# Performance work log

Hardware: AMD Instinct MI355X
Metric: run time of the kernel (lower is better)

The kernel has to match this reference:

```python
import jax, jax.numpy as jnp
import numpy as np

H = 4      # num_heads
C = 64     # attention_num_c
C_Z = 128  # num_in_c (pair rep channels)
C_T = 64   # num_in_c_kv (template pair channels)


def setup_inputs() -> dict:
    key = jax.random.key(0)
    ks = jax.random.split(key, 7)
    B, T, R = 1, 4, 384
    z2d = jax.random.normal(ks[0], (B, R, R, C_Z), dtype=jnp.float32)
    t2d = jax.random.normal(ks[1], (B, T, R, R, C_T), dtype=jnp.float32)
    s = 0.02
    Wq = jax.random.normal(ks[2], (C_Z, H * C), dtype=jnp.float32) * s
    Wk = jax.random.normal(ks[3], (C_T, H * C), dtype=jnp.float32) * s
    Wv = jax.random.normal(ks[4], (C_T, H * C), dtype=jnp.float32) * s
    Wo = jax.random.normal(ks[5], (H * C, C_Z), dtype=jnp.float32) * s
    bo = jax.random.normal(ks[6], (C_Z,), dtype=jnp.float32) * s
    return {"z2d": z2d, "t2d": t2d, "Wq": Wq, "Wk": Wk, "Wv": Wv, "Wo": Wo, "bo": bo}


def reference(z2d, t2d, Wq, Wk, Wv, Wo, bo):
    B, R = z2d.shape[0], z2d.shape[-2]
    T = t2d.shape[1]
    P = R * R  # residue-pair axis
    # query: one query per residue pair
    zq = z2d.reshape(B, P, 1, C_Z)
    # templates become the key/value axis per residue pair
    tkv = jnp.transpose(t2d, (0, 2, 3, 1, 4)).reshape(B, P, T, C_T)
    q = (zq @ Wq).reshape(B, P, 1, H, C) * (C ** -0.5)
    k = (tkv @ Wk).reshape(B, P, T, H, C)
    v = (tkv @ Wv).reshape(B, P, T, H, C)
    logits = jnp.einsum('bpqhc,bpkhc->bphqk', q, k)  # [B,P,H,1,T]
    weights = jax.nn.softmax(logits, axis=-1)
    weighted_avg = jnp.einsum('bphqk,bpkhc->bpqhc', weights, v)  # [B,P,1,H,C]
    out = weighted_avg.reshape(B, P, 1, H * C) @ Wo + bo
    return out.reshape(B, R, R, C_Z)
```

## Files before the change

kernel.cpp:

```cpp
#include <hip/hip_runtime.h>


#define R_   384
#define P_   (R_ * R_)
#define NBLK (P_ / 64)

typedef __attribute__((ext_vector_type(8))) short  short8;
typedef __attribute__((ext_vector_type(4))) float  f32x4;

__device__ __forceinline__ unsigned short f2bf(float f) {
  unsigned u = __float_as_uint(f);
  unsigned r = ((u >> 16) & 1u) + 0x7FFFu;
  return (unsigned short)((u + r) >> 16);
}
__device__ __forceinline__ float bf2f(unsigned short s) {
  return __uint_as_float(((unsigned)s) << 16);
}
__device__ __forceinline__ int swz(int p, int c) {
  return p * 256 + ((((c >> 3) ^ (p & 31)) << 3) | (c & 7));
}

__global__ void prep_kernel(const float* __restrict__ Wq, const float* __restrict__ Wk,
                            const float* __restrict__ Wv, const float* __restrict__ Wo,
                            unsigned short* __restrict__ AbarT,
                            unsigned short* __restrict__ MbarT) {
  int tid = blockIdx.x * blockDim.x + threadIdx.x;
  if (tid < 256 * 128) {
    int n = tid >> 7, i = tid & 127;
    int h = n >> 6, j = n & 63;
    const float* wq = Wq + i * 256 + h * 64;
    const float* wk = Wk + j * 256 + h * 64;
    float acc = 0.f;
#pragma unroll 8
    for (int c = 0; c < 64; ++c) acc += wq[c] * wk[c];
    AbarT[n * 128 + i] = f2bf(acc * 0.125f);
  } else {
    int t2 = tid - 256 * 128;
    int o = t2 >> 8, k = t2 & 255;
    int h = k >> 6, j = k & 63;
    const float* wv = Wv + j * 256 + h * 64;
    const float* wo = Wo + (h * 64) * 128 + o;
    float acc = 0.f;
#pragma unroll 8
    for (int c = 0; c < 64; ++c) acc += wv[c] * wo[c * 128];
    MbarT[o * 256 + k] = f2bf(acc);
  }
}

__global__ __launch_bounds__(256, 2) void attn_kernel(
    const float* __restrict__ z2d, const float* __restrict__ t2d,
    const unsigned short* __restrict__ AbarT, const unsigned short* __restrict__ MbarT,
    const float* __restrict__ bo, float* __restrict__ out) {
  __shared__ __align__(16) unsigned short sT[64 * 256];
  __shared__ __align__(16) unsigned short sG[64 * 256];

  const int tid = threadIdx.x;
  const int P0  = blockIdx.x * 64;

#pragma unroll
  for (int it = 0; it < 16; ++it) {
    int f  = it * 256 + tid;
    int t  = f >> 10;
    int rr = f & 1023;
    int p  = rr >> 4;
    int j4 = (rr & 15) << 2;
    const float4 v = *(const float4*)(t2d + (size_t)(t * P_ + P0 + p) * 64 + j4);
    ushort4 pk;
    pk.x = f2bf(v.x); pk.y = f2bf(v.y); pk.z = f2bf(v.z); pk.w = f2bf(v.w);
    *(ushort4*)(sT + swz(p, t * 64 + j4)) = pk;
  }

  const int wv_  = tid >> 6;
  const int lane = tid & 63;
  const int l = lane & 15;
  const int q = lane >> 4;

  f32x4 acc[16];
#pragma unroll
  for (int i = 0; i < 16; ++i) acc[i] = f32x4{0.f, 0.f, 0.f, 0.f};
  const float* zrow = z2d + (size_t)(P0 + wv_ * 16 + l) * 128;
#pragma unroll
  for (int kk = 0; kk < 4; ++kk) {
    float4 za = *(const float4*)(zrow + kk * 32 + q * 8);
    float4 zb = *(const float4*)(zrow + kk * 32 + q * 8 + 4);
    short8 af;
    af[0] = (short)f2bf(za.x); af[1] = (short)f2bf(za.y);
    af[2] = (short)f2bf(za.z); af[3] = (short)f2bf(za.w);
    af[4] = (short)f2bf(zb.x); af[5] = (short)f2bf(zb.y);
    af[6] = (short)f2bf(zb.z); af[7] = (short)f2bf(zb.w);
    const unsigned short* bbase = AbarT + l * 128 + kk * 32 + q * 8;
#pragma unroll
    for (int nt = 0; nt < 16; ++nt) {
      short8 bf = *(const short8*)(bbase + nt * 2048);
      acc[nt] = __builtin_amdgcn_mfma_f32_16x16x32_bf16(af, bf, acc[nt], 0, 0, 0);
    }
  }
#pragma unroll
  for (int nt = 0; nt < 16; ++nt) {
    int c = nt * 16 + l;
#pragma unroll
    for (int r = 0; r < 4; ++r) {
      int p = wv_ * 16 + q * 4 + r;
      sG[swz(p, c)] = f2bf(acc[nt][r]);
    }
  }
  __syncthreads();

  {
    const int p = tid & 63;
    const int h = tid >> 6;
    float lg0 = 0.f, lg1 = 0.f, lg2 = 0.f, lg3 = 0.f;
#pragma unroll
    for (int jb = 0; jb < 64; jb += 4) {
      ushort4 g4 = *(const ushort4*)(sG + swz(p, h * 64 + jb));
      float g0 = bf2f(g4.x), g1 = bf2f(g4.y), g2 = bf2f(g4.z), g3 = bf2f(g4.w);
      ushort4 k0 = *(const ushort4*)(sT + swz(p, jb));
      ushort4 k1 = *(const ushort4*)(sT + swz(p, 64 + jb));
      ushort4 k2 = *(const ushort4*)(sT + swz(p, 128 + jb));
      ushort4 k3 = *(const ushort4*)(sT + swz(p, 192 + jb));
      lg0 += g0 * bf2f(k0.x) + g1 * bf2f(k0.y) + g2 * bf2f(k0.z) + g3 * bf2f(k0.w);
      lg1 += g0 * bf2f(k1.x) + g1 * bf2f(k1.y) + g2 * bf2f(k1.z) + g3 * bf2f(k1.w);
      lg2 += g0 * bf2f(k2.x) + g1 * bf2f(k2.y) + g2 * bf2f(k2.z) + g3 * bf2f(k2.w);
      lg3 += g0 * bf2f(k3.x) + g1 * bf2f(k3.y) + g2 * bf2f(k3.z) + g3 * bf2f(k3.w);
    }
    float mx = fmaxf(fmaxf(lg0, lg1), fmaxf(lg2, lg3));
    float e0 = __expf(lg0 - mx), e1 = __expf(lg1 - mx);
    float e2 = __expf(lg2 - mx), e3 = __expf(lg3 - mx);
    float inv = 1.f / (e0 + e1 + e2 + e3);
    e0 *= inv; e1 *= inv; e2 *= inv; e3 *= inv;
#pragma unroll
    for (int jb = 0; jb < 64; jb += 4) {
      ushort4 k0 = *(const ushort4*)(sT + swz(p, jb));
      ushort4 k1 = *(const ushort4*)(sT + swz(p, 64 + jb));
      ushort4 k2 = *(const ushort4*)(sT + swz(p, 128 + jb));
      ushort4 k3 = *(const ushort4*)(sT + swz(p, 192 + jb));
      ushort4 sv;
      sv.x = f2bf(e0 * bf2f(k0.x) + e1 * bf2f(k1.x) + e2 * bf2f(k2.x) + e3 * bf2f(k3.x));
      sv.y = f2bf(e0 * bf2f(k0.y) + e1 * bf2f(k1.y) + e2 * bf2f(k2.y) + e3 * bf2f(k3.y));
      sv.z = f2bf(e0 * bf2f(k0.z) + e1 * bf2f(k1.z) + e2 * bf2f(k2.z) + e3 * bf2f(k3.z));
      sv.w = f2bf(e0 * bf2f(k0.w) + e1 * bf2f(k1.w) + e2 * bf2f(k2.w) + e3 * bf2f(k3.w));
      *(ushort4*)(sG + swz(p, h * 64 + jb)) = sv;
    }
  }
  __syncthreads();

  f32x4 acc2[4][2];
#pragma unroll
  for (int mt = 0; mt < 4; ++mt) {
    acc2[mt][0] = f32x4{0.f, 0.f, 0.f, 0.f};
    acc2[mt][1] = f32x4{0.f, 0.f, 0.f, 0.f};
  }
#pragma unroll
  for (int kk = 0; kk < 8; ++kk) {
    const unsigned short* mb = MbarT + (size_t)(wv_ * 32 + l) * 256 + kk * 32 + q * 8;
    short8 b0 = *(const short8*)(mb);
    short8 b1 = *(const short8*)(mb + 16 * 256);
#pragma unroll
    for (int mt = 0; mt < 4; ++mt) {
      const int p  = mt * 16 + l;
      const int cb = kk * 32 + q * 8;
      short8 af2 = *(const short8*)(sG + p * 256 + (((cb >> 3) ^ (p & 31)) << 3));
      acc2[mt][0] = __builtin_amdgcn_mfma_f32_16x16x32_bf16(af2, b0, acc2[mt][0], 0, 0, 0);
      acc2[mt][1] = __builtin_amdgcn_mfma_f32_16x16x32_bf16(af2, b1, acc2[mt][1], 0, 0, 0);
    }
  }
  const float bo0 = bo[wv_ * 32 + l];
  const float bo1 = bo[wv_ * 32 + 16 + l];
#pragma unroll
  for (int mt = 0; mt < 4; ++mt) {
#pragma unroll
    for (int r = 0; r < 4; ++r) {
      size_t row = (size_t)(P0 + mt * 16 + q * 4 + r);
      out[row * 128 + wv_ * 32 + l]      = acc2[mt][0][r] + bo0;
      out[row * 128 + wv_ * 32 + 16 + l] = acc2[mt][1][r] + bo1;
    }
  }
}

extern "C" void kernel_launch(void* const* d_in, const int* in_sizes, int n_in,
                              void* d_out, int out_size, void* d_ws, size_t ws_size,
                              hipStream_t stream) {
  const float* z2d = (const float*)d_in[0];
  const float* t2d = (const float*)d_in[1];
  const float* Wq  = (const float*)d_in[2];
  const float* Wk  = (const float*)d_in[3];
  const float* Wv  = (const float*)d_in[4];
  const float* Wo  = (const float*)d_in[5];
  const float* bo  = (const float*)d_in[6];

  unsigned short* AbarT = (unsigned short*)d_ws;
  unsigned short* MbarT = AbarT + 256 * 128;
  float* out = (float*)d_out;

  hipLaunchKernelGGL(prep_kernel, dim3(256), dim3(256), 0, stream,
                     Wq, Wk, Wv, Wo, AbarT, MbarT);
  hipLaunchKernelGGL(attn_kernel, dim3(NBLK), dim3(256), 0, stream,
                     z2d, t2d, AbarT, MbarT, bo, out);
}
```

Before: 354.9 us.

## Halve per-block pair tile to 32 and remap waves for higher occupancy

Each block now handles 32 residue pairs instead of 64, which halves shared memory and accumulator registers so launch bounds can request four blocks per CU. The wave-to-tile mapping in both MFMA GEMMs is rearranged so each wave covers one 16-row M tile and half the N dimension. The softmax stage splits each pair's channel reduction across two lanes, using 16-byte LDS accesses and a shuffle to combine partial sums. In exchange, the weight matrices are reread from global/L2 by twice as many blocks, and there is more per-block overhead.

```diff
diff --git a/kernel.cpp b/kernel.cpp
--- a/kernel.cpp
+++ b/kernel.cpp
@@ -3,7 +3,8 @@
 
 #define R_   384
 #define P_   (R_ * R_)
-#define NBLK (P_ / 64)
+#define PB   32
+#define NBLK (P_ / PB)
 
 typedef __attribute__((ext_vector_type(8))) short  short8;
 typedef __attribute__((ext_vector_type(4))) float  f32x4;
@@ -47,21 +48,21 @@
   }
 }
 
-__global__ __launch_bounds__(256, 2) void attn_kernel(
+__global__ __launch_bounds__(256, 4) void attn_kernel(
     const float* __restrict__ z2d, const float* __restrict__ t2d,
     const unsigned short* __restrict__ AbarT, const unsigned short* __restrict__ MbarT,
     const float* __restrict__ bo, float* __restrict__ out) {
-  __shared__ __align__(16) unsigned short sT[64 * 256];
-  __shared__ __align__(16) unsigned short sG[64 * 256];
+  __shared__ __align__(16) unsigned short sT[PB * 256];
+  __shared__ __align__(16) unsigned short sG[PB * 256];
 
   const int tid = threadIdx.x;
-  const int P0  = blockIdx.x * 64;
-
-#pragma unroll
-  for (int it = 0; it < 16; ++it) {
+  const int P0  = blockIdx.x * PB;
+
+#pragma unroll
+  for (int it = 0; it < 8; ++it) {
     int f  = it * 256 + tid;
-    int t  = f >> 10;
-    int rr = f & 1023;
+    int t  = f >> 9;
+    int rr = f & 511;
     int p  = rr >> 4;
     int j4 = (rr & 15) << 2;
     const float4 v = *(const float4*)(t2d + (size_t)(t * P_ + P0 + p) * 64 + j4);
@@ -74,11 +75,13 @@
   const int lane = tid & 63;
   const int l = lane & 15;
   const int q = lane >> 4;
-
-  f32x4 acc[16];
-#pragma unroll
-  for (int i = 0; i < 16; ++i) acc[i] = f32x4{0.f, 0.f, 0.f, 0.f};
-  const float* zrow = z2d + (size_t)(P0 + wv_ * 16 + l) * 128;
+  const int mt = wv_ & 1;
+  const int nh = wv_ >> 1;
+
+  f32x4 acc[8];
+#pragma unroll
+  for (int i = 0; i < 8; ++i) acc[i] = f32x4{0.f, 0.f, 0.f, 0.f};
+  const float* zrow = z2d + (size_t)(P0 + mt * 16 + l) * 128;
 #pragma unroll
   for (int kk = 0; kk < 4; ++kk) {
     float4 za = *(const float4*)(zrow + kk * 32 + q * 8);
@@ -88,91 +91,98 @@
     af[2] = (short)f2bf(za.z); af[3] = (short)f2bf(za.w);
     af[4] = (short)f2bf(zb.x); af[5] = (short)f2bf(zb.y);
     af[6] = (short)f2bf(zb.z); af[7] = (short)f2bf(zb.w);
-    const unsigned short* bbase = AbarT + l * 128 + kk * 32 + q * 8;
-#pragma unroll
-    for (int nt = 0; nt < 16; ++nt) {
-      short8 bf = *(const short8*)(bbase + nt * 2048);
-      acc[nt] = __builtin_amdgcn_mfma_f32_16x16x32_bf16(af, bf, acc[nt], 0, 0, 0);
-    }
-  }
-#pragma unroll
-  for (int nt = 0; nt < 16; ++nt) {
-    int c = nt * 16 + l;
+    const unsigned short* bbase = AbarT + (nh * 8) * 2048 + l * 128 + kk * 32 + q * 8;
+#pragma unroll
+    for (int i = 0; i < 8; ++i) {
+      short8 bf = *(const short8*)(bbase + i * 2048);
+      acc[i] = __builtin_amdgcn_mfma_f32_16x16x32_bf16(af, bf, acc[i], 0, 0, 0);
+    }
+  }
+#pragma unroll
+  for (int i = 0; i < 8; ++i) {
+    int c = (nh * 8 + i) * 16 + l;
 #pragma unroll
     for (int r = 0; r < 4; ++r) {
-      int p = wv_ * 16 + q * 4 + r;
-      sG[swz(p, c)] = f2bf(acc[nt][r]);
+      int p = mt * 16 + q * 4 + r;
+      sG[swz(p, c)] = f2bf(acc[i][r]);
     }
   }
   __syncthreads();
 
   {
-    const int p = tid & 63;
-    const int h = tid >> 6;
+    const int p    = lane >> 1;
+    const int half = lane & 1;
+    const int h    = wv_;
+    const int c0   = half * 32;
     float lg0 = 0.f, lg1 = 0.f, lg2 = 0.f, lg3 = 0.f;
 #pragma unroll
-    for (int jb = 0; jb < 64; jb += 4) {
-      ushort4 g4 = *(const ushort4*)(sG + swz(p, h * 64 + jb));
-      float g0 = bf2f(g4.x), g1 = bf2f(g4.y), g2 = bf2f(g4.z), g3 = bf2f(g4.w);
-      ushort4 k0 = *(const ushort4*)(sT + swz(p, jb));
-      ushort4 k1 = *(const ushort4*)(sT + swz(p, 64 + jb));
-      ushort4 k2 = *(const ushort4*)(sT + swz(p, 128 + jb));
-      ushort4 k3 = *(const ushort4*)(sT + swz(p, 192 + jb));
-      lg0 += g0 * bf2f(k0.x) + g1 * bf2f(k0.y) + g2 * bf2f(k0.z) + g3 * bf2f(k0.w);
-      lg1 += g0 * bf2f(k1.x) + g1 * bf2f(k1.y) + g2 * bf2f(k1.z) + g3 * bf2f(k1.w);
-      lg2 += g0 * bf2f(k2.x) + g1 * bf2f(k2.y) + g2 * bf2f(k2.z) + g3 * bf2f(k2.w);
-      lg3 += g0 * bf2f(k3.x) + g1 * bf2f(k3.y) + g2 * bf2f(k3.z) + g3 * bf2f(k3.w);
-    }
+    for (int jj = 0; jj < 4; ++jj) {
+      const int cc = c0 + jj * 8;
+      short8 g8 = *(const short8*)(sG + swz(p, h * 64 + cc));
+      short8 k0 = *(const short8*)(sT + swz(p, cc));
+      short8 k1 = *(const short8*)(sT + swz(p, 64 + cc));
+      short8 k2 = *(const short8*)(sT + swz(p, 128 + cc));
+      short8 k3 = *(const short8*)(sT + swz(p, 192 + cc));
+#pragma unroll
+      for (int e = 0; e < 8; ++e) {
+        float g = bf2f((unsigned short)g8[e]);
+        lg0 += g * bf2f((unsigned short)k0[e]);
+        lg1 += g * bf2f((unsigned short)k1[e]);
+        lg2 += g * bf2f((unsigned short)k2[e]);
+        lg3 += g * bf2f((unsigned short)k3[e]);
+      }
+    }
+    lg0 += __shfl_xor(lg0, 1);
+    lg1 += __shfl_xor(lg1, 1);
+    lg2 += __shfl_xor(lg2, 1);
+    lg3 += __shfl_xor(lg3, 1);
     float mx = fmaxf(fmaxf(lg0, lg1), fmaxf(lg2, lg3));
     float e0 = __expf(lg0 - mx), e1 = __expf(lg1 - mx);
     float e2 = __expf(lg2 - mx), e3 = __expf(lg3 - mx);
     float inv = 1.f / (e0 + e1 + e2 + e3);
     e0 *= inv; e1 *= inv; e2 *= inv; e3 *= inv;
 #pragma unroll
-    for (int jb = 0; jb < 64; jb += 4) {
-      ushort4 k0 = *(const ushort4*)(sT + swz(p, jb));
-      ushort4 k1 = *(const ushort4*)(sT + swz(p, 64 + jb));
-      ushort4 k2 = *(const ushort4*)(sT + swz(p, 128 + jb));
-      ushort4 k3 = *(const ushort4*)(sT + swz(p, 192 + jb));
-      ushort4 sv;
-      sv.x = f2bf(e0 * bf2f(k0.x) + e1 * bf2f(k1.x) + e2 * bf2f(k2.x) + e3 * bf2f(k3.x));
-      sv.y = f2bf(e0 * bf2f(k0.y) + e1 * bf2f(k1.y) + e2 * bf2f(k2.y) + e3 * bf2f(k3.y));
-      sv.z = f2bf(e0 * bf2f(k0.z) + e1 * bf2f(k1.z) + e2 * bf2f(k2.z) + e3 * bf2f(k3.z));
-      sv.w = f2bf(e0 * bf2f(k0.w) + e1 * bf2f(k1.w) + e2 * bf2f(k2.w) + e3 * bf2f(k3.w));
-      *(ushort4*)(sG + swz(p, h * 64 + jb)) = sv;
+    for (int jj = 0; jj < 4; ++jj) {
+      const int cc = c0 + jj * 8;
+      short8 k0 = *(const short8*)(sT + swz(p, cc));
+      short8 k1 = *(const short8*)(sT + swz(p, 64 + cc));
+      short8 k2 = *(const short8*)(sT + swz(p, 128 + cc));
+      short8 k3 = *(const short8*)(sT + swz(p, 192 + cc));
+      short8 sv;
+#pragma unroll
+      for (int e = 0; e < 8; ++e) {
+        float s = e0 * bf2f((unsigned short)k0[e]) + e1 * bf2f((unsigned short)k1[e])
+                + e2 * bf2f((unsigned short)k2[e]) + e3 * bf2f((unsigned short)k3[e]);
+        sv[e] = (short)f2bf(s);
+      }
+      *(short8*)(sG + swz(p, h * 64 + cc)) = sv;
     }
   }
   __syncthreads();
 
-  f32x4 acc2[4][2];
-#pragma unroll
-  for (int mt = 0; mt < 4; ++mt) {
-    acc2[mt][0] = f32x4{0.f, 0.f, 0.f, 0.f};
-    acc2[mt][1] = f32x4{0.f, 0.f, 0.f, 0.f};
-  }
+  f32x4 acc2[4];
+#pragma unroll
+  for (int i = 0; i < 4; ++i) acc2[i] = f32x4{0.f, 0.f, 0.f, 0.f};
 #pragma unroll
   for (int kk = 0; kk < 8; ++kk) {
-    const unsigned short* mb = MbarT + (size_t)(wv_ * 32 + l) * 256 + kk * 32 + q * 8;
-    short8 b0 = *(const short8*)(mb);
-    short8 b1 = *(const short8*)(mb + 16 * 256);
-#pragma unroll
-    for (int mt = 0; mt < 4; ++mt) {
-      const int p  = mt * 16 + l;
-      const int cb = kk * 32 + q * 8;
-      short8 af2 = *(const short8*)(sG + p * 256 + (((cb >> 3) ^ (p & 31)) << 3));
-      acc2[mt][0] = __builtin_amdgcn_mfma_f32_16x16x32_bf16(af2, b0, acc2[mt][0], 0, 0, 0);
-      acc2[mt][1] = __builtin_amdgcn_mfma_f32_16x16x32_bf16(af2, b1, acc2[mt][1], 0, 0, 0);
-    }
-  }
-  const float bo0 = bo[wv_ * 32 + l];
-  const float bo1 = bo[wv_ * 32 + 16 + l];
-#pragma unroll
-  for (int mt = 0; mt < 4; ++mt) {
+    const int p  = mt * 16 + l;
+    const int cb = kk * 32 + q * 8;
+    short8 af2 = *(const short8*)(sG + p * 256 + (((cb >> 3) ^ (p & 31)) << 3));
+    const unsigned short* mb = MbarT + (size_t)(nh * 64 + l) * 256 + kk * 32 + q * 8;
+#pragma unroll
+    for (int i = 0; i < 4; ++i) {
+      short8 bf = *(const short8*)(mb + i * 16 * 256);
+      acc2[i] = __builtin_amdgcn_mfma_f32_16x16x32_bf16(af2, bf, acc2[i], 0, 0, 0);
+    }
+  }
+#pragma unroll
+  for (int i = 0; i < 4; ++i) {
+    const int o   = nh * 64 + i * 16 + l;
+    const float b = bo[o];
 #pragma unroll
     for (int r = 0; r < 4; ++r) {
       size_t row = (size_t)(P0 + mt * 16 + q * 4 + r);
-      out[row * 128 + wv_ * 32 + l]      = acc2[mt][0][r] + bo0;
-      out[row * 128 + wv_ * 32 + 16 + l] = acc2[mt][1][r] + bo1;
+      out[row * 128 + o] = acc2[i][r] + b;
     }
   }
 }
```

Result: slower. 394.4 us (+11.1%).

## Convert attention kernel to persistent blocks with double-buffered software pipeline

Applied to the files above, without the earlier changes.

Replaces the one-tile-per-block launch with 256 persistent 512-thread blocks, each looping over 18 tiles of 32 pairs. Abar is staged once in LDS and the Mbar fragments are held in registers, so per-tile weight reloads from global memory go away. Each iteration prefetches the next tile's t2d and z2d into registers and overlaps the previous tile's output GEMM with the current tile's work through double-buffered LDS. It also uses packed bf16 conversion instructions, wider LDS accesses with shuffle reductions, and 128KB of dynamic shared memory, which raises register pressure and may limit occupancy.

```diff
diff --git a/kernel.cpp b/kernel.cpp
--- a/kernel.cpp
+++ b/kernel.cpp
@@ -1,12 +1,16 @@
 #include <hip/hip_runtime.h>
 
 
-#define R_   384
-#define P_   (R_ * R_)
-#define NBLK (P_ / 64)
+#define R_    384
+#define P_    (R_ * R_)
+#define PB    32
+#define NPB   256
+#define NT_   18
 
 typedef __attribute__((ext_vector_type(8))) short  short8;
 typedef __attribute__((ext_vector_type(4))) float  f32x4;
+
+union S8U { short8 s8; unsigned u[4]; };
 
 __device__ __forceinline__ unsigned short f2bf(float f) {
   unsigned u = __float_as_uint(f);
@@ -16,9 +20,18 @@
 __device__ __forceinline__ float bf2f(unsigned short s) {
   return __uint_as_float(((unsigned)s) << 16);
 }
+__device__ __forceinline__ unsigned cvtpk(float lo, float hi) {
+  unsigned d;
+  asm("v_cvt_pk_bf16_f32 %0, %1, %2" : "=v"(d) : "v"(lo), "v"(hi));
+  return d;
+}
 __device__ __forceinline__ int swz(int p, int c) {
   return p * 256 + ((((c >> 3) ^ (p & 31)) << 3) | (c & 7));
 }
+#define BAR() do { \
+    asm volatile("s_waitcnt lgkmcnt(0)\ns_barrier" ::: "memory"); \
+    __builtin_amdgcn_sched_barrier(0); \
+  } while (0)
 
 __global__ void prep_kernel(const float* __restrict__ Wq, const float* __restrict__ Wk,
                             const float* __restrict__ Wv, const float* __restrict__ Wo,
@@ -47,134 +60,221 @@
   }
 }
 
-__global__ __launch_bounds__(256, 2) void attn_kernel(
+__global__ __launch_bounds__(512, 2) void attn_kernel(
     const float* __restrict__ z2d, const float* __restrict__ t2d,
     const unsigned short* __restrict__ AbarT, const unsigned short* __restrict__ MbarT,
     const float* __restrict__ bo, float* __restrict__ out) {
-  __shared__ __align__(16) unsigned short sT[64 * 256];
-  __shared__ __align__(16) unsigned short sG[64 * 256];
-
-  const int tid = threadIdx.x;
-  const int P0  = blockIdx.x * 64;
-
-#pragma unroll
-  for (int it = 0; it < 16; ++it) {
-    int f  = it * 256 + tid;
-    int t  = f >> 10;
-    int rr = f & 1023;
-    int p  = rr >> 4;
-    int j4 = (rr & 15) << 2;
-    const float4 v = *(const float4*)(t2d + (size_t)(t * P_ + P0 + p) * 64 + j4);
-    ushort4 pk;
-    pk.x = f2bf(v.x); pk.y = f2bf(v.y); pk.z = f2bf(v.z); pk.w = f2bf(v.w);
-    *(ushort4*)(sT + swz(p, t * 64 + j4)) = pk;
-  }
-
+  extern __shared__ unsigned short smem[];
+  unsigned short* sAbar = smem;
+  unsigned short* sT    = smem + 32768;
+  unsigned short* sG    = smem + 49152;
+
+  const int tid  = threadIdx.x;
   const int wv_  = tid >> 6;
   const int lane = tid & 63;
   const int l = lane & 15;
   const int q = lane >> 4;
-
-  f32x4 acc[16];
-#pragma unroll
-  for (int i = 0; i < 16; ++i) acc[i] = f32x4{0.f, 0.f, 0.f, 0.f};
-  const float* zrow = z2d + (size_t)(P0 + wv_ * 16 + l) * 128;
-#pragma unroll
-  for (int kk = 0; kk < 4; ++kk) {
-    float4 za = *(const float4*)(zrow + kk * 32 + q * 8);
-    float4 zb = *(const float4*)(zrow + kk * 32 + q * 8 + 4);
-    short8 af;
-    af[0] = (short)f2bf(za.x); af[1] = (short)f2bf(za.y);
-    af[2] = (short)f2bf(za.z); af[3] = (short)f2bf(za.w);
-    af[4] = (short)f2bf(zb.x); af[5] = (short)f2bf(zb.y);
-    af[6] = (short)f2bf(zb.z); af[7] = (short)f2bf(zb.w);
-    const unsigned short* bbase = AbarT + l * 128 + kk * 32 + q * 8;
-#pragma unroll
-    for (int nt = 0; nt < 16; ++nt) {
-      short8 bf = *(const short8*)(bbase + nt * 2048);
-      acc[nt] = __builtin_amdgcn_mfma_f32_16x16x32_bf16(af, bf, acc[nt], 0, 0, 0);
-    }
-  }
-#pragma unroll
-  for (int nt = 0; nt < 16; ++nt) {
-    int c = nt * 16 + l;
+  const int mt = wv_ & 1;
+  const int ng = wv_ >> 1;
+
+  int sOffS[4], sOffD[4];
+#pragma unroll
+  for (int k2 = 0; k2 < 4; ++k2) {
+    int f = k2 * 512 + tid, t = f >> 9, rr = f & 511;
+    int p2 = rr >> 4, j4 = (rr & 15) << 2;
+    sOffS[k2] = t * (P_ * 64) + p2 * 64 + j4;
+    sOffD[k2] = swz(p2, t * 64 + j4);
+  }
+  const int zoff = (mt * 16 + l) * 128;
+  const int p2g  = mt * 16 + l;
+  const int ap = tid >> 4, asub = tid & 15;
+  const int ah = asub >> 2, au = asub & 3;
+  const int aoG0 = swz(ap, ah * 64 + au * 16);
+  const int aoG1 = swz(ap, ah * 64 + au * 16 + 8);
+  int aoK[4][2];
+#pragma unroll
+  for (int t = 0; t < 4; ++t) {
+    aoK[t][0] = swz(ap, t * 64 + au * 16);
+    aoK[t][1] = swz(ap, t * 64 + au * 16 + 8);
+  }
+
+#pragma unroll
+  for (int k2 = 0; k2 < 8; ++k2) {
+    int id = k2 * 512 + tid, n = id >> 4, blk = id & 15;
+    short8 v = *(const short8*)(AbarT + n * 128 + blk * 8);
+    *(short8*)(sAbar + n * 128 + ((blk ^ (n & 15)) << 3)) = v;
+  }
+  short8 mb0[8], mb1[8];
+#pragma unroll
+  for (int kk = 0; kk < 8; ++kk) {
+    mb0[kk] = *(const short8*)(MbarT + (size_t)((ng * 2)     * 16 + l) * 256 + kk * 32 + q * 8);
+    mb1[kk] = *(const short8*)(MbarT + (size_t)((ng * 2 + 1) * 16 + l) * 256 + kk * 32 + q * 8);
+  }
+  const float bo0 = bo[(ng * 2) * 16 + l];
+  const float bo1 = bo[(ng * 2 + 1) * 16 + l];
+
+  float4 st0, st1, st2, st3;
+  float4 zpA[8], zpB[8];
+  {
+    const size_t P00 = (size_t)blockIdx.x * PB;
+    const float* tb = t2d + P00 * 64;
+    st0 = *(const float4*)(tb + sOffS[0]);
+    st1 = *(const float4*)(tb + sOffS[1]);
+    st2 = *(const float4*)(tb + sOffS[2]);
+    st3 = *(const float4*)(tb + sOffS[3]);
+    const float* zr = z2d + P00 * 128 + zoff;
+#pragma unroll
+    for (int kk = 0; kk < 4; ++kk) {
+      zpA[2 * kk]     = *(const float4*)(zr + kk * 32 + q * 8);
+      zpA[2 * kk + 1] = *(const float4*)(zr + kk * 32 + q * 8 + 4);
+    }
+  }
+  BAR();
+
+  auto gemm2 = [&](const unsigned short* sGp, size_t P0p) {
+    f32x4 a20 = f32x4{0.f, 0.f, 0.f, 0.f};
+    f32x4 a21 = f32x4{0.f, 0.f, 0.f, 0.f};
+#pragma unroll
+    for (int kk = 0; kk < 8; ++kk) {
+      short8 af2 = *(const short8*)(sGp + p2g * 256 + (((kk * 4 + q) ^ (p2g & 31)) << 3));
+      a20 = __builtin_amdgcn_mfma_f32_16x16x32_bf16(af2, mb0[kk], a20, 0, 0, 0);
+      a21 = __builtin_amdgcn_mfma_f32_16x16x32_bf16(af2, mb1[kk], a21, 0, 0, 0);
+    }
+    const size_t rb = (P0p + (size_t)(mt * 16 + q * 4)) * 128;
 #pragma unroll
     for (int r = 0; r < 4; ++r) {
-      int p = wv_ * 16 + q * 4 + r;
-      sG[swz(p, c)] = f2bf(acc[nt][r]);
-    }
-  }
-  __syncthreads();
-
-  {
-    const int p = tid & 63;
-    const int h = tid >> 6;
+      out[rb + r * 128 + ng * 32 + l]      = a20[r] + bo0;
+      out[rb + r * 128 + ng * 32 + 16 + l] = a21[r] + bo1;
+    }
+  };
+
+  auto attention = [&](const unsigned short* sTc, unsigned short* sGc) {
+    short8 g0 = *(const short8*)(sGc + aoG0);
+    short8 g1 = *(const short8*)(sGc + aoG1);
+    short8 kc00 = *(const short8*)(sTc + aoK[0][0]);
+    short8 kc01 = *(const short8*)(sTc + aoK[0][1]);
+    short8 kc10 = *(const short8*)(sTc + aoK[1][0]);
+    short8 kc11 = *(const short8*)(sTc + aoK[1][1]);
+    short8 kc20 = *(const short8*)(sTc + aoK[2][0]);
+    short8 kc21 = *(const short8*)(sTc + aoK[2][1]);
+    short8 kc30 = *(const short8*)(sTc + aoK[3][0]);
+    short8 kc31 = *(const short8*)(sTc + aoK[3][1]);
     float lg0 = 0.f, lg1 = 0.f, lg2 = 0.f, lg3 = 0.f;
 #pragma unroll
-    for (int jb = 0; jb < 64; jb += 4) {
-      ushort4 g4 = *(const ushort4*)(sG + swz(p, h * 64 + jb));
-      float g0 = bf2f(g4.x), g1 = bf2f(g4.y), g2 = bf2f(g4.z), g3 = bf2f(g4.w);
-      ushort4 k0 = *(const ushort4*)(sT + swz(p, jb));
-      ushort4 k1 = *(const ushort4*)(sT + swz(p, 64 + jb));
-      ushort4 k2 = *(const ushort4*)(sT + swz(p, 128 + jb));
-      ushort4 k3 = *(const ushort4*)(sT + swz(p, 192 + jb));
-      lg0 += g0 * bf2f(k0.x) + g1 * bf2f(k0.y) + g2 * bf2f(k0.z) + g3 * bf2f(k0.w);
-      lg1 += g0 * bf2f(k1.x) + g1 * bf2f(k1.y) + g2 * bf2f(k1.z) + g3 * bf2f(k1.w);
-      lg2 += g0 * bf2f(k2.x) + g1 * bf2f(k2.y) + g2 * bf2f(k2.z) + g3 * bf2f(k2.w);
-      lg3 += g0 * bf2f(k3.x) + g1 * bf2f(k3.y) + g2 * bf2f(k3.z) + g3 * bf2f(k3.w);
-    }
-    float mx = fmaxf(fmaxf(lg0, lg1), fmaxf(lg2, lg3));
+    for (int e = 0; e < 8; ++e) {
+      const float ga = bf2f((unsigned short)g0[e]);
+      const float gb = bf2f((unsigned short)g1[e]);
+      lg0 += ga * bf2f((unsigned short)kc00[e]) + gb * bf2f((unsigned short)kc01[e]);
+      lg1 += ga * bf2f((unsigned short)kc10[e]) + gb * bf2f((unsigned short)kc11[e]);
+      lg2 += ga * bf2f((unsigned short)kc20[e]) + gb * bf2f((unsigned short)kc21[e]);
+      lg3 += ga * bf2f((unsigned short)kc30[e]) + gb * bf2f((unsigned short)kc31[e]);
+    }
+    lg0 += __shfl_xor(lg0, 1); lg0 += __shfl_xor(lg0, 2);
+    lg1 += __shfl_xor(lg1, 1); lg1 += __shfl_xor(lg1, 2);
+    lg2 += __shfl_xor(lg2, 1); lg2 += __shfl_xor(lg2, 2);
+    lg3 += __shfl_xor(lg3, 1); lg3 += __shfl_xor(lg3, 2);
+    const float mx = fmaxf(fmaxf(lg0, lg1), fmaxf(lg2, lg3));
     float e0 = __expf(lg0 - mx), e1 = __expf(lg1 - mx);
     float e2 = __expf(lg2 - mx), e3 = __expf(lg3 - mx);
-    float inv = 1.f / (e0 + e1 + e2 + e3);
+    const float inv = 1.f / (e0 + e1 + e2 + e3);
     e0 *= inv; e1 *= inv; e2 *= inv; e3 *= inv;
-#pragma unroll
-    for (int jb = 0; jb < 64; jb += 4) {
-      ushort4 k0 = *(const ushort4*)(sT + swz(p, jb));
-      ushort4 k1 = *(const ushort4*)(sT + swz(p, 64 + jb));
-      ushort4 k2 = *(const ushort4*)(sT + swz(p, 128 + jb));
-      ushort4 k3 = *(const ushort4*)(sT + swz(p, 192 + jb));
-      ushort4 sv;
-      sv.x = f2bf(e0 * bf2f(k0.x) + e1 * bf2f(k1.x) + e2 * bf2f(k2.x) + e3 * bf2f(k3.x));
-      sv.y = f2bf(e0 * bf2f(k0.y) + e1 * bf2f(k1.y) + e2 * bf2f(k2.y) + e3 * bf2f(k3.y));
-      sv.z = f2bf(e0 * bf2f(k0.z) + e1 * bf2f(k1.z) + e2 * bf2f(k2.z) + e3 * bf2f(k3.z));
-      sv.w = f2bf(e0 * bf2f(k0.w) + e1 * bf2f(k1.w) + e2 * bf2f(k2.w) + e3 * bf2f(k3.w));
-      *(ushort4*)(sG + swz(p, h * 64 + jb)) = sv;
-    }
-  }
-  __syncthreads();
-
-  f32x4 acc2[4][2];
-#pragma unroll
-  for (int mt = 0; mt < 4; ++mt) {
-    acc2[mt][0] = f32x4{0.f, 0.f, 0.f, 0.f};
-    acc2[mt][1] = f32x4{0.f, 0.f, 0.f, 0.f};
-  }
-#pragma unroll
-  for (int kk = 0; kk < 8; ++kk) {
-    const unsigned short* mb = MbarT + (size_t)(wv_ * 32 + l) * 256 + kk * 32 + q * 8;
-    short8 b0 = *(const short8*)(mb);
-    short8 b1 = *(const short8*)(mb + 16 * 256);
-#pragma unroll
-    for (int mt = 0; mt < 4; ++mt) {
-      const int p  = mt * 16 + l;
-      const int cb = kk * 32 + q * 8;
-      short8 af2 = *(const short8*)(sG + p * 256 + (((cb >> 3) ^ (p & 31)) << 3));
-      acc2[mt][0] = __builtin_amdgcn_mfma_f32_16x16x32_bf16(af2, b0, acc2[mt][0], 0, 0, 0);
-      acc2[mt][1] = __builtin_amdgcn_mfma_f32_16x16x32_bf16(af2, b1, acc2[mt][1], 0, 0, 0);
-    }
-  }
-  const float bo0 = bo[wv_ * 32 + l];
-  const float bo1 = bo[wv_ * 32 + 16 + l];
-#pragma unroll
-  for (int mt = 0; mt < 4; ++mt) {
-#pragma unroll
-    for (int r = 0; r < 4; ++r) {
-      size_t row = (size_t)(P0 + mt * 16 + q * 4 + r);
-      out[row * 128 + wv_ * 32 + l]      = acc2[mt][0][r] + bo0;
-      out[row * 128 + wv_ * 32 + 16 + l] = acc2[mt][1][r] + bo1;
-    }
-  }
+    S8U sv;
+#pragma unroll
+    for (int j2 = 0; j2 < 4; ++j2) {
+      float s0 = e0 * bf2f((unsigned short)kc00[2 * j2])     + e1 * bf2f((unsigned short)kc10[2 * j2])
+               + e2 * bf2f((unsigned short)kc20[2 * j2])     + e3 * bf2f((unsigned short)kc30[2 * j2]);
+      float s1 = e0 * bf2f((unsigned short)kc00[2 * j2 + 1]) + e1 * bf2f((unsigned short)kc10[2 * j2 + 1])
+               + e2 * bf2f((unsigned short)kc20[2 * j2 + 1]) + e3 * bf2f((unsigned short)kc30[2 * j2 + 1]);
+      sv.u[j2] = cvtpk(s0, s1);
+    }
+    *(short8*)(sGc + aoG0) = sv.s8;
+#pragma unroll
+    for (int j2 = 0; j2 < 4; ++j2) {
+      float s0 = e0 * bf2f((unsigned short)kc01[2 * j2])     + e1 * bf2f((unsigned short)kc11[2 * j2])
+               + e2 * bf2f((unsigned short)kc21[2 * j2])     + e3 * bf2f((unsigned short)kc31[2 * j2]);
+      float s1 = e0 * bf2f((unsigned short)kc01[2 * j2 + 1]) + e1 * bf2f((unsigned short)kc11[2 * j2 + 1])
+               + e2 * bf2f((unsigned short)kc21[2 * j2 + 1]) + e3 * bf2f((unsigned short)kc31[2 * j2 + 1]);
+      sv.u[j2] = cvtpk(s0, s1);
+    }
+    *(short8*)(sGc + aoG1) = sv.s8;
+  };
+
+#define HALF_BODY(IT_, CUR_, ZPC, ZPN, DO_G2, DO_PF)                           \
+  {                                                                            \
+    const size_t P0 = (size_t)blockIdx.x * PB + (size_t)(IT_) * (NPB * PB);    \
+    unsigned short* sTc = sT + (CUR_) * 8192;                                  \
+    unsigned short* sGc = sG + (CUR_) * 8192;                                  \
+    const unsigned short* sGp = sG + (1 - (CUR_)) * 8192;                      \
+                \
+    { uint2 w;                                                                 \
+      w.x = cvtpk(st0.x, st0.y); w.y = cvtpk(st0.z, st0.w);                    \
+      *(uint2*)(sTc + sOffD[0]) = w;                                           \
+      w.x = cvtpk(st1.x, st1.y); w.y = cvtpk(st1.z, st1.w);                    \
+      *(uint2*)(sTc + sOffD[1]) = w;                                           \
+      w.x = cvtpk(st2.x, st2.y); w.y = cvtpk(st2.z, st2.w);                    \
+      *(uint2*)(sTc + sOffD[2]) = w;                                           \
+      w.x = cvtpk(st3.x, st3.y); w.y = cvtpk(st3.z, st3.w);                    \
+      *(uint2*)(sTc + sOffD[3]) = w; }                                         \
+    \
+    if (DO_PF) {                                                               \
+      const float* tb = t2d + (P0 + NPB * PB) * 64;                            \
+      st0 = *(const float4*)(tb + sOffS[0]);                                   \
+      st1 = *(const float4*)(tb + sOffS[1]);                                   \
+      st2 = *(const float4*)(tb + sOffS[2]);                                   \
+      st3 = *(const float4*)(tb + sOffS[3]);                                   \
+      const float* zr = z2d + (P0 + NPB * PB) * 128 + zoff;                    \
+      _Pragma("unroll")                                                        \
+      for (int kk = 0; kk < 4; ++kk) {                                         \
+        ZPN[2 * kk]     = *(const float4*)(zr + kk * 32 + q * 8);              \
+        ZPN[2 * kk + 1] = *(const float4*)(zr + kk * 32 + q * 8 + 4);          \
+      }                                                                        \
+    }                                                                          \
+                                                  \
+    if (DO_G2) gemm2(sGp, P0 - (size_t)(NPB * PB));                            \
+                   \
+    {                                                                          \
+      f32x4 a1[4];                                                             \
+      _Pragma("unroll")                                                        \
+      for (int i = 0; i < 4; ++i) a1[i] = f32x4{0.f, 0.f, 0.f, 0.f};           \
+      _Pragma("unroll")                                                        \
+      for (int kk = 0; kk < 4; ++kk) {                                         \
+        S8U af;                                                                \
+        af.u[0] = cvtpk(ZPC[2 * kk].x,     ZPC[2 * kk].y);                     \
+        af.u[1] = cvtpk(ZPC[2 * kk].z,     ZPC[2 * kk].w);                     \
+        af.u[2] = cvtpk(ZPC[2 * kk + 1].x, ZPC[2 * kk + 1].y);                 \
+        af.u[3] = cvtpk(ZPC[2 * kk + 1].z, ZPC[2 * kk + 1].w);                 \
+        _Pragma("unroll")                                                      \
+        for (int i = 0; i < 4; ++i) {                                          \
+          const int n = (ng * 4 + i) * 16 + l;                                 \
+          short8 bf = *(const short8*)(sAbar + n * 128 + (((kk * 4 + q) ^ l) << 3)); \
+          a1[i] = __builtin_amdgcn_mfma_f32_16x16x32_bf16(af.s8, bf, a1[i], 0, 0, 0); \
+        }                                                                      \
+      }                                                                        \
+      _Pragma("unroll")                                                        \
+      for (int i = 0; i < 4; ++i) {                                            \
+        const int c = (ng * 4 + i) * 16 + l;                                   \
+        _Pragma("unroll")                                                      \
+        for (int r = 0; r < 4; ++r) {                                          \
+          const int p2 = mt * 16 + q * 4 + r;                                  \
+          sGc[swz(p2, c)] = f2bf(a1[i][r]);    \
+        }                                                                      \
+      }                                                                        \
+    }                                                                          \
+    BAR();                                                                     \
+                                                    \
+    attention(sTc, sGc);                                                       \
+    BAR();                                                                     \
+  }
+
+#pragma unroll 1
+  for (int j = 0; j < NT_ / 2; ++j) {
+    const int it0 = 2 * j;
+    HALF_BODY(it0,     0, zpA, zpB, (it0 > 0), true);
+    HALF_BODY(it0 + 1, 1, zpB, zpA, true,      (j < NT_ / 2 - 1));
+  }
+#undef HALF_BODY
+
+  gemm2(sG + 8192, (size_t)blockIdx.x * PB + (size_t)(NT_ - 1) * (NPB * PB));
 }
 
 extern "C" void kernel_launch(void* const* d_in, const int* in_sizes, int n_in,
@@ -192,8 +292,15 @@
   unsigned short* MbarT = AbarT + 256 * 128;
   float* out = (float*)d_out;
 
+  static bool attr_set = false;
+  if (!attr_set) {
+    (void)hipFuncSetAttribute((const void*)attn_kernel,
+                              hipFuncAttributeMaxDynamicSharedMemorySize, 131072);
+    attr_set = true;
+  }
+
   hipLaunchKernelGGL(prep_kernel, dim3(256), dim3(256), 0, stream,
                      Wq, Wk, Wv, Wo, AbarT, MbarT);
-  hipLaunchKernelGGL(attn_kernel, dim3(NBLK), dim3(256), 0, stream,
+  hipLaunchKernelGGL(attn_kernel, dim3(NPB), dim3(512), 131072, stream,
                      z2d, t2d, AbarT, MbarT, bo, out);
 }
```

Result: slower. 482.6 us (+36.0%).
